# Kernel tuning notes

Hardware: AMD Instinct MI355X
Metric: run time of the kernel (lower is better)

## Reference

```python
import jax, jax.numpy as jnp
import numpy as np
from jax import lax

D_STATE = 16
D_CONV = 4
EXPAND = 2

def silu(x):
    return x * jax.nn.sigmoid(x)

def layernorm(x, w, b, eps=1e-5):
    mu = jnp.mean(x, axis=-1, keepdims=True)
    var = jnp.mean(jnp.square(x - mu), axis=-1, keepdims=True)
    return (x - mu) * lax.rsqrt(var + eps) * w + b

def adaln(x, t, W, b):
    # x: (B, N, C), t: (B, C); modulation = Linear(SiLU(t)) -> (B, 2C)
    m = silu(t) @ W.T + b
    scale, shift = jnp.split(m, 2, axis=-1)
    return x * (1.0 + scale[:, None, :]) + shift[:, None, :]

def mamba(x, W_in, conv_w, conv_b, W_x, W_dt, b_dt, A_log, D_p, W_out):
    # x: (B, L, D)
    B, L, D = x.shape
    di = conv_w.shape[0]           # d_inner = 2*D
    n = A_log.shape[1]             # d_state
    dtr = W_dt.shape[1]            # dt_rank
    xz = x @ W_in.T                # (B, L, 2*di)
    xi, z = jnp.split(xz, 2, axis=-1)
    # depthwise causal conv1d along L
    xt = jnp.transpose(xi, (0, 2, 1))                      # (B, di, L)
    xc = lax.conv_general_dilated(
        xt, conv_w[:, None, :], window_strides=(1,),
        padding=[(D_CONV - 1, 0)], feature_group_count=di,
        dimension_numbers=('NCH', 'OIH', 'NCH'))
    xc = silu(jnp.transpose(xc, (0, 2, 1)) + conv_b)       # (B, L, di)
    x_dbl = xc @ W_x.T                                     # (B, L, dtr+2n)
    dt, Bm, Cm = jnp.split(x_dbl, [dtr, dtr + n], axis=-1)
    delta = jax.nn.softplus(dt @ W_dt.T + b_dt)            # (B, L, di)
    A = -jnp.exp(A_log)                                    # (di, n)
    def step(h, inp):
        d_t, B_t, C_t, x_t = inp                           # (B,di),(B,n),(B,n),(B,di)
        dA = jnp.exp(d_t[..., None] * A)                   # (B, di, n)
        h = dA * h + (d_t * x_t)[..., None] * B_t[:, None, :]
        y = jnp.sum(h * C_t[:, None, :], axis=-1)          # (B, di)
        return h, y
    h0 = jnp.zeros((B, di, n), dtype=x.dtype)
    xs = (jnp.transpose(delta, (1, 0, 2)), jnp.transpose(Bm, (1, 0, 2)),
          jnp.transpose(Cm, (1, 0, 2)), jnp.transpose(xc, (1, 0, 2)))
    _, ys = lax.scan(step, h0, xs)                         # (L, B, di)
    y = jnp.transpose(ys, (1, 0, 2)) + xc * D_p
    y = y * silu(z)
    return y @ W_out.T

def _forward(query, diff_ts, p):
    outs = []
    n_layers = p['W_in'].shape[0]
    for i in range(n_layers):
        # cross-attn layer (Mamba) with AdaLN + residual + LN
        aq = adaln(query, diff_ts, p['attn_ada_W'][i], p['attn_ada_b'][i])
        attn = mamba(aq, p['W_in'][i], p['conv_w'][i], p['conv_b'][i],
                     p['W_x'][i], p['W_dt'][i], p['b_dt'][i],
                     p['A_log'][i], p['D_p'][i], p['W_out'][i])
        query = layernorm(query + attn, p['attn_ln_w'][i], p['attn_ln_b'][i])
        # FFN with AdaLN + residual + LN
        xf = adaln(query, diff_ts, p['ff_ada_W'][i], p['ff_ada_b'][i])
        h = jax.nn.relu(xf @ p['ff_W1'][i].T + p['ff_b1'][i])
        out = h @ p['ff_W2'][i].T + p['ff_b2'][i]
        query = layernorm(xf + out, p['ff_ln_w'][i], p['ff_ln_b'][i])
        outs.append(query)
    return tuple(outs)

def setup_inputs() -> dict:
    key = jax.random.key(0)
    B, L, D, NL = 4, 4096, 256, 4
    di = EXPAND * D
    n = D_STATE
    dtr = max(1, int(np.ceil(D / 16)))
    ks = iter(jax.random.split(key, 64))
    r = lambda shape, s=0.02: (s * jax.random.normal(next(ks), shape)).astype(jnp.float32)
    inp = {
        'query': jax.random.normal(next(ks), (B, L, D), dtype=jnp.float32),
        'value': jax.random.normal(next(ks), (B, L, D), dtype=jnp.float32),
        'diff_ts': jax.random.normal(next(ks), (B, D), dtype=jnp.float32),
        'W_in': r((NL, 2 * di, D)),
        'conv_w': r((NL, di, D_CONV), 0.2),
        'conv_b': r((NL, di)),
        'W_x': r((NL, dtr + 2 * n, di)),
        'W_dt': r((NL, di, dtr), 0.1),
        'b_dt': r((NL, di), 0.1),
        'A_log': jnp.log(jnp.broadcast_to(jnp.arange(1, n + 1, dtype=jnp.float32), (NL, di, n))),
        'D_p': jnp.ones((NL, di), dtype=jnp.float32),
        'W_out': r((NL, D, di)),
        'attn_ada_W': r((NL, 2 * D, D)),
        'attn_ada_b': r((NL, 2 * D)),
        'attn_ln_w': jnp.ones((NL, D), dtype=jnp.float32),
        'attn_ln_b': jnp.zeros((NL, D), dtype=jnp.float32),
        'ff_W1': r((NL, D, D)),
        'ff_b1': jnp.zeros((NL, D), dtype=jnp.float32),
        'ff_W2': r((NL, D, D)),
        'ff_b2': jnp.zeros((NL, D), dtype=jnp.float32),
        'ff_ln_w': jnp.ones((NL, D), dtype=jnp.float32),
        'ff_ln_b': jnp.zeros((NL, D), dtype=jnp.float32),
        'ff_ada_W': r((NL, 2 * D, D)),
        'ff_ada_b': r((NL, 2 * D)),
    }
    return inp

def reference(query, value, diff_ts, W_in, conv_w, conv_b, W_x, W_dt, b_dt,
              A_log, D_p, W_out, attn_ada_W, attn_ada_b, attn_ln_w, attn_ln_b,
              ff_W1, ff_b1, ff_W2, ff_b2, ff_ln_w, ff_ln_b, ff_ada_W, ff_ada_b):
    p = dict(W_in=W_in, conv_w=conv_w, conv_b=conv_b, W_x=W_x, W_dt=W_dt,
             b_dt=b_dt, A_log=A_log, D_p=D_p, W_out=W_out,
             attn_ada_W=attn_ada_W, attn_ada_b=attn_ada_b,
             attn_ln_w=attn_ln_w, attn_ln_b=attn_ln_b,
             ff_W1=ff_W1, ff_b1=ff_b1, ff_W2=ff_W2, ff_b2=ff_b2,
             ff_ln_w=ff_ln_w, ff_ln_b=ff_ln_b,
             ff_ada_W=ff_ada_W, ff_ada_b=ff_ada_b)
    return _forward(query, diff_ts, p)
```

## Files before the change

### kernel.cpp

```cpp
#include <hip/hip_runtime.h>
#include <hip/hip_bf16.h>

#define B_   4
#define L_   4096
#define D_   256
#define DI_  512
#define BL_  (B_*L_)
#define NL_  4
#define NC_  32
#define LC_  128

typedef __hip_bfloat16 bf16;
typedef __attribute__((ext_vector_type(8))) short short8;
typedef __attribute__((ext_vector_type(4))) short short4v;
typedef __attribute__((ext_vector_type(4))) float f32x4;

__device__ __forceinline__ float b2f(bf16 v) { return __bfloat162float(v); }
__device__ __forceinline__ float sh2f(short s) { bf16 h = *(bf16*)&s; return __bfloat162float(h); }
__device__ __forceinline__ float ldx(const void* p, size_t i, int isf32) {
  return isf32 ? ((const float*)p)[i] : b2f(((const bf16*)p)[i]);
}
__device__ __forceinline__ short f2s(float f) {
  bf16 h = __float2bfloat16(f);
  return *(short*)&h;
}

__global__ void k_probe(const unsigned* __restrict__ alog, int* __restrict__ flg) {
  if (threadIdx.x == 0) *flg = (alog[0] == 0u) ? 1 : 0;
}

__global__ __launch_bounds__(256) void k_cvt1(const void* __restrict__ src, size_t off,
                                              bf16* __restrict__ dst, int n,
                                              const int* __restrict__ flg) {
  int isf32 = *flg;
  int i = blockIdx.x * 256 + threadIdx.x;
  if (i < n) dst[i] = __float2bfloat16(ldx(src, off + i, isf32));
}

__global__ __launch_bounds__(256) void k_preA(const void* __restrict__ Alog,
                                              float* __restrict__ Ac,
                                              const int* __restrict__ flg) {
  int isf32 = *flg;
  int i = blockIdx.x * 256 + threadIdx.x;
  if (i < NL_ * 8192) Ac[i] = -__expf(ldx(Alog, (size_t)i, isf32)) * 1.44269504f;
}

__global__ __launch_bounds__(256) void k_mod(const void* __restrict__ t,
                                             const void* __restrict__ Wa, const void* __restrict__ ba,
                                             const void* __restrict__ Wf, const void* __restrict__ bfb,
                                             float* __restrict__ m,
                                             const int* __restrict__ flg) {
  int isf32 = *flg;
  int wt = blockIdx.x * 4 + (threadIdx.x >> 6);
  int lane = threadIdx.x & 63;
  int layer = wt >> 12;
  int w = wt & 4095;
  int o = w & 511;
  int b = (w >> 9) & 3;
  int which = w >> 11;
  const void* W  = which ? Wf : Wa;
  const void* bb = which ? bfb : ba;
  size_t wbase = (size_t)layer * 512 * 256 + (size_t)o * 256;
  float acc = 0.f;
#pragma unroll
  for (int j = 0; j < 4; ++j) {
    int k = lane + 64 * j;
    float tv = ldx(t, b * D_ + k, isf32);
    float s = tv / (1.f + __expf(-tv));
    acc = fmaf(s, ldx(W, wbase + k, isf32), acc);
  }
#pragma unroll
  for (int m2 = 32; m2 >= 1; m2 >>= 1) acc += __shfl_xor(acc, m2, 64);
  if (lane == 0) m[(layer << 12) + w] = acc + ldx(bb, (size_t)layer * 512 + o, isf32);
}

__global__ __launch_bounds__(256) void k_cvt_adaln(const void* __restrict__ qin,
                                                   bf16* __restrict__ q16,
                                                   bf16* __restrict__ oada,
                                                   const float* __restrict__ mod,
                                                   const int* __restrict__ flg) {
  int isf32 = *flg;
  int i = blockIdx.x * 256 + threadIdx.x;
  int c = i & (D_ - 1);
  int b = i >> 20;
  float v = ldx(qin, (size_t)i, isf32);
  q16[i] = __float2bfloat16(v);
  oada[i] = __float2bfloat16(fmaf(v, 1.f + mod[b * 512 + c], mod[b * 512 + 256 + c]));
}

__device__ __forceinline__ void gld_lds16(bf16* lds, const bf16* g) {
  __builtin_amdgcn_global_load_lds((const __attribute__((address_space(1))) unsigned int*)g,
                                   (__attribute__((address_space(3))) unsigned int*)lds,
                                   16, 0, 0);
}

__global__ __launch_bounds__(256) void k_gemm_t(const bf16* __restrict__ A,
                                                const bf16* __restrict__ W,
                                                const void* __restrict__ bias, size_t belem0,
                                                bf16* __restrict__ outB, bf16* __restrict__ out2,
                                                int N, int K, int relu,
                                                const int* __restrict__ flg) {
  __shared__ __align__(16) bf16 As[8192], Bs[8192];
  int isf32 = *flg;
  int tid = threadIdx.x;
  int lane = tid & 63, wave = tid >> 6;
  int tn = N >> 7;
  int m0 = (blockIdx.x / tn) << 7;
  int n0 = (blockIdx.x % tn) << 7;
  int wm = (wave >> 1) << 6, wn = (wave & 1) << 6;
  int r = lane & 15, q = lane >> 4;
  f32x4 acc[4][4];
#pragma unroll
  for (int a = 0; a < 4; ++a)
#pragma unroll
    for (int b = 0; b < 4; ++b) acc[a][b] = (f32x4){0.f, 0.f, 0.f, 0.f};
  const bf16* Ab = A + (size_t)m0 * K;
  const bf16* Wb = W + (size_t)n0 * K;
  for (int k0 = 0; k0 < K; k0 += 64) {
    __syncthreads();
#pragma unroll
    for (int j = 0; j < 4; ++j) {
      int g = tid + j * 256;
      int row = g >> 3;
      int slot = (g & 7) ^ (row & 7);
      gld_lds16(As + (size_t)g * 8, Ab + (size_t)row * K + k0 + slot * 8);
      gld_lds16(Bs + (size_t)g * 8, Wb + (size_t)row * K + k0 + slot * 8);
    }
    __syncthreads();
#pragma unroll
    for (int kk = 0; kk < 2; ++kk) {
      short8 af[4], bv[4];
#pragma unroll
      for (int f = 0; f < 4; ++f) {
        int ra = wm + f * 16 + r;
        af[f] = *(const short8*)((const short*)As + ra * 64 + (((kk * 4 + q) ^ (ra & 7)) << 3));
        int rb = wn + f * 16 + r;
        bv[f] = *(const short8*)((const short*)Bs + rb * 64 + (((kk * 4 + q) ^ (rb & 7)) << 3));
      }
#pragma unroll
      for (int i2 = 0; i2 < 4; ++i2)
#pragma unroll
        for (int j2 = 0; j2 < 4; ++j2)
          acc[i2][j2] = __builtin_amdgcn_mfma_f32_16x16x32_bf16(af[i2], bv[j2], acc[i2][j2], 0, 0, 0);
    }
  }
#pragma unroll
  for (int j2 = 0; j2 < 4; ++j2) {
    int col = n0 + wn + j2 * 16 + r;
    float bb = bias ? ldx(bias, belem0 + col, isf32) : 0.f;
#pragma unroll
    for (int i2 = 0; i2 < 4; ++i2) {
      int rw = m0 + wm + i2 * 16 + q * 4;
#pragma unroll
      for (int j = 0; j < 4; ++j) {
        float v = acc[i2][j2][j] + bb;
        if (relu) v = fmaxf(v, 0.f);
        bf16* dst; size_t idx;
        if (out2) {
          int hh = N >> 1;
          if (col < hh) { dst = outB; idx = (size_t)(rw + j) * hh + col; }
          else          { dst = out2; idx = (size_t)(rw + j) * hh + col - hh; }
        } else { dst = outB; idx = (size_t)(rw + j) * N + col; }
        dst[idx] = __float2bfloat16(v);
      }
    }
  }
}

__global__ __launch_bounds__(256) void k_gemm(const bf16* __restrict__ A,
                                              const bf16* __restrict__ W,
                                              bf16* __restrict__ outB,
                                              int N, int K) {
  int wave = threadIdx.x >> 6, lane = threadIdx.x & 63;
  int t = blockIdx.x * 4 + wave;
  int tn = N >> 4;
  int m0 = (t / tn) << 4;
  int n0 = (t % tn) << 4;
  int r = lane & 15, q = lane >> 4;
  const short* Ar = (const short*)A + (size_t)(m0 + r) * K + q * 8;
  const short* Wr = (const short*)W + (size_t)(n0 + r) * K + q * 8;
  f32x4 acc = {0.f, 0.f, 0.f, 0.f};
  for (int k = 0; k < K; k += 32)
    acc = __builtin_amdgcn_mfma_f32_16x16x32_bf16(*(const short8*)(Ar + k),
                                                  *(const short8*)(Wr + k), acc, 0, 0, 0);
  int col = n0 + r;
#pragma unroll
  for (int j = 0; j < 4; ++j)
    outB[(size_t)(m0 + q * 4 + j) * N + col] = __float2bfloat16(acc[j]);
}

__global__ __launch_bounds__(256) void k_conv(const bf16* __restrict__ Xi,
                                              const void* __restrict__ cw, const void* __restrict__ cb,
                                              bf16* __restrict__ xc16, int layer,
                                              const int* __restrict__ flg) {
  int isf32 = *flg;
  int i = blockIdx.x * 256 + threadIdx.x;
  int c8 = (i & 63) << 3;
  int row = i >> 6;
  int l = row & (L_ - 1);
  size_t cwb = (size_t)layer * 2048 + (size_t)c8 * 4;
  float acc[8];
#pragma unroll
  for (int e = 0; e < 8; ++e) acc[e] = ldx(cb, (size_t)layer * 512 + c8 + e, isf32);
#pragma unroll
  for (int j = 0; j < 4; ++j) {
    int ll = l - 3 + j;
    if (ll >= 0) {
      short8 xv = *(const short8*)((const short*)Xi + (size_t)(row - 3 + j) * 512 + c8);
#pragma unroll
      for (int e = 0; e < 8; ++e) {
        acc[e] = fmaf(ldx(cw, cwb + e * 4 + j, isf32), sh2f(xv[e]), acc[e]);
      }
    }
  }
  short8 o;
#pragma unroll
  for (int e = 0; e < 8; ++e) {
    float s = acc[e] * (1.f / (1.f + __expf(-acc[e])));
    o[e] = f2s(s);
  }
  *(short8*)((short*)xc16 + (size_t)row * 512 + c8) = o;
}

__global__ __launch_bounds__(256) void k_xpose(const bf16* __restrict__ src,
                                               bf16* __restrict__ dst) {
  __shared__ bf16 t[64][66];
  int bid = blockIdx.x;
  int ct = bid & 7;
  int lt = (bid >> 3) & 63;
  int b  = bid >> 9;
  int l0 = lt * 64, c0 = ct * 64;
  int tx = threadIdx.x & 63;
  int ty = threadIdx.x >> 6;
#pragma unroll
  for (int j = 0; j < 16; ++j) {
    int l = ty + j * 4;
    t[l][tx] = src[(size_t)(b * L_ + l0 + l) * 512 + c0 + tx];
  }
  __syncthreads();
#pragma unroll
  for (int j = 0; j < 16; ++j) {
    int c = ty + j * 4;
    dst[(size_t)(b * 512 + c0 + c) * L_ + l0 + tx] = t[tx][c];
  }
}

__global__ __launch_bounds__(256) void k_scan1_t(const bf16* __restrict__ Tx,
                                                 const bf16* __restrict__ xdbl,
                                                 const void* __restrict__ Wdt,
                                                 const void* __restrict__ bdt,
                                                 const float* __restrict__ Ac, int layer,
                                                 bf16* __restrict__ Pscr, float* __restrict__ Hscr,
                                                 const int* __restrict__ flg) {
  __shared__ __align__(16) bf16 rowbuf[LC_ * 48];
  __shared__ bf16 dlbuf[64 * 130];
  int isf32 = *flg;
  int tid = blockIdx.x * 256 + threadIdx.x;
  int nh = tid & 3;
  int d  = (tid >> 2) & 511;
  int t2 = tid >> 11;
  int c  = t2 & (NC_ - 1);
  int b  = t2 >> 5;
  int dl = (threadIdx.x >> 2) & 63;
  const bf16* rowg = xdbl + (size_t)(b * L_ + c * LC_) * 48;
#pragma unroll
  for (int j = 0; j < 3; ++j) {
    int o = threadIdx.x * 8 + j * 2048;
    *(short8*)(rowbuf + o) = *(const short8*)(rowg + o);
  }
  __syncthreads();
  {
    float w[16];
    size_t wb = (size_t)layer * 8192 + (size_t)d * 16;
#pragma unroll
    for (int k = 0; k < 16; ++k) w[k] = ldx(Wdt, wb + k, isf32);
    float dbias = ldx(bdt, (size_t)layer * 512 + d, isf32);
    for (int jl = 0; jl < 32; ++jl) {
      int l = nh * 32 + jl;
      const bf16* rr = rowbuf + l * 48;
      short8 t0 = *(const short8*)rr;
      short8 t1 = *(const short8*)(rr + 8);
      float acc = dbias;
#pragma unroll
      for (int k = 0; k < 8; ++k) acc = fmaf(sh2f(t0[k]), w[k], acc);
#pragma unroll
      for (int k = 0; k < 8; ++k) acc = fmaf(sh2f(t1[k]), w[k + 8], acc);
      dlbuf[dl * 130 + l] = __float2bfloat16(fmaxf(acc, 0.f) + log1pf(__expf(-fabsf(acc))));
    }
  }
  __syncthreads();
  const float* ap = Ac + (size_t)layer * 8192 + (size_t)d * 16 + nh * 4;
  float av[4], h[4], P[4];
#pragma unroll
  for (int n = 0; n < 4; ++n) { av[n] = ap[n]; h[n] = 0.f; P[n] = 1.f; }
  const bf16* xp = Tx + (size_t)(b * 512 + d) * L_ + c * LC_;
  const bf16* dlp = dlbuf + dl * 130;
  for (int l8 = 0; l8 < LC_; l8 += 8) {
    short8 xv8 = *(const short8*)(xp + l8);
#pragma unroll
    for (int e = 0; e < 8; ++e) {
      int l = l8 + e;
      float dv = b2f(dlp[l]);
      short4v bm = *(const short4v*)(rowbuf + l * 48 + 16 + nh * 4);
      float u = dv * sh2f(xv8[e]);
#pragma unroll
      for (int n = 0; n < 4; ++n) {
        float da = exp2f(dv * av[n]);
        h[n] = fmaf(da, h[n], u * sh2f(bm[n]));
        P[n] *= da;
      }
    }
  }
  int s = (b * 512 + d) * 16 + nh * 4;
  bf16* pp = Pscr + (size_t)c * 32768 + s;
  float* hp = Hscr + (size_t)c * 32768 + s;
#pragma unroll
  for (int n = 0; n < 4; ++n) { pp[n] = __float2bfloat16(P[n]); hp[n] = h[n]; }
}

__global__ __launch_bounds__(256) void k_scan2(const bf16* __restrict__ Pscr,
                                               float* __restrict__ Hscr) {
  int s = blockIdx.x * 256 + threadIdx.x;
  float hin = 0.f;
  for (int c = 0; c < NC_; ++c) {
    float P  = b2f(Pscr[(size_t)c * 32768 + s]);
    float he = Hscr[(size_t)c * 32768 + s];
    Hscr[(size_t)c * 32768 + s] = hin;
    hin = fmaf(P, hin, he);
  }
}

__global__ __launch_bounds__(256) void k_scan3_t(bf16* __restrict__ Tx,
                                                 const bf16* __restrict__ xdbl,
                                                 const void* __restrict__ Wdt,
                                                 const void* __restrict__ bdt,
                                                 const float* __restrict__ Ac, int layer,
                                                 const float* __restrict__ Hscr,
                                                 const int* __restrict__ flg) {
  __shared__ __align__(16) bf16 rowbuf[LC_ * 48];
  __shared__ bf16 dlbuf[64 * 130];
  int isf32 = *flg;
  int tid = blockIdx.x * 256 + threadIdx.x;
  int nh = tid & 3;
  int d  = (tid >> 2) & 511;
  int t2 = tid >> 11;
  int c  = t2 & (NC_ - 1);
  int b  = t2 >> 5;
  int dl = (threadIdx.x >> 2) & 63;
  const bf16* rowg = xdbl + (size_t)(b * L_ + c * LC_) * 48;
#pragma unroll
  for (int j = 0; j < 3; ++j) {
    int o = threadIdx.x * 8 + j * 2048;
    *(short8*)(rowbuf + o) = *(const short8*)(rowg + o);
  }
  __syncthreads();
  {
    float w[16];
    size_t wb = (size_t)layer * 8192 + (size_t)d * 16;
#pragma unroll
    for (int k = 0; k < 16; ++k) w[k] = ldx(Wdt, wb + k, isf32);
    float dbias = ldx(bdt, (size_t)layer * 512 + d, isf32);
    for (int jl = 0; jl < 32; ++jl) {
      int l = nh * 32 + jl;
      const bf16* rr = rowbuf + l * 48;
      short8 t0 = *(const short8*)rr;
      short8 t1 = *(const short8*)(rr + 8);
      float acc = dbias;
#pragma unroll
      for (int k = 0; k < 8; ++k) acc = fmaf(sh2f(t0[k]), w[k], acc);
#pragma unroll
      for (int k = 0; k < 8; ++k) acc = fmaf(sh2f(t1[k]), w[k + 8], acc);
      dlbuf[dl * 130 + l] = __float2bfloat16(fmaxf(acc, 0.f) + log1pf(__expf(-fabsf(acc))));
    }
  }
  __syncthreads();
  const float* ap = Ac + (size_t)layer * 8192 + (size_t)d * 16 + nh * 4;
  int s = (b * 512 + d) * 16 + nh * 4;
  const float* hp = Hscr + (size_t)c * 32768 + s;
  float av[4], h[4];
#pragma unroll
  for (int n = 0; n < 4; ++n) { av[n] = ap[n]; h[n] = hp[n]; }
  bf16* xp = Tx + (size_t)(b * 512 + d) * L_ + c * LC_;
  const bf16* dlp = dlbuf + dl * 130;
  for (int l8 = 0; l8 < LC_; l8 += 8) {
    short8 xv8 = *(const short8*)(xp + l8);
    short8 y8;
#pragma unroll
    for (int e = 0; e < 8; ++e) {
      int l = l8 + e;
      float dv = b2f(dlp[l]);
      short4v bm = *(const short4v*)(rowbuf + l * 48 + 16 + nh * 4);
      short4v cm = *(const short4v*)(rowbuf + l * 48 + 32 + nh * 4);
      float u = dv * sh2f(xv8[e]);
      float y = 0.f;
#pragma unroll
      for (int n = 0; n < 4; ++n) {
        float da = exp2f(dv * av[n]);
        h[n] = fmaf(da, h[n], u * sh2f(bm[n]));
        y = fmaf(h[n], sh2f(cm[n]), y);
      }
      y += __shfl_xor(y, 1, 64);
      y += __shfl_xor(y, 2, 64);
      y8[e] = f2s(y);
    }
    if (nh == 0) *(short8*)(xp + l8) = y8;
  }
}

__global__ __launch_bounds__(256) void k_gate_t(const bf16* __restrict__ yT,
                                                bf16* __restrict__ xc,
                                                const bf16* __restrict__ Z,
                                                const void* __restrict__ Dp, int layer,
                                                const int* __restrict__ flg) {
  __shared__ bf16 t[64][66];
  int isf32 = *flg;
  int bid = blockIdx.x;
  int ct = bid & 7;
  int lt = (bid >> 3) & 63;
  int b  = bid >> 9;
  int l0 = lt * 64, c0 = ct * 64;
  int tx = threadIdx.x & 63;
  int ty = threadIdx.x >> 6;
#pragma unroll
  for (int j = 0; j < 16; ++j) {
    int dd = ty + j * 4;
    t[dd][tx] = yT[(size_t)(b * 512 + c0 + dd) * L_ + l0 + tx];
  }
  __syncthreads();
  float dpv = ldx(Dp, (size_t)layer * 512 + c0 + tx, isf32);
#pragma unroll
  for (int j = 0; j < 16; ++j) {
    int l = ty + j * 4;
    size_t row = (size_t)(b * L_ + l0 + l);
    float y  = b2f(t[tx][l]);
    float xcv = b2f(xc[row * 512 + c0 + tx]);
    float zv = b2f(Z[row * 512 + c0 + tx]);
    float v = fmaf(xcv, dpv, y);
    xc[row * 512 + c0 + tx] = __float2bfloat16(v * zv / (1.f + __expf(-zv)));
  }
}

__global__ __launch_bounds__(256) void k_delta(const bf16* __restrict__ xdbl,
                                               const void* __restrict__ Wdt, const void* __restrict__ bdt,
                                               bf16* __restrict__ dly, int layer,
                                               const int* __restrict__ flg) {
  __shared__ float Wls[256 * 17];
  int isf32 = *flg;
  int i = blockIdx.x * 256 + threadIdx.x;
  int d = i & (DI_ - 1);
  int row = i >> 9;
  int d0 = (blockIdx.x & 1) * 256;
  size_t wbase = (size_t)layer * 512 * 16 + (size_t)d0 * 16;
#pragma unroll
  for (int jj = 0; jj < 16; ++jj) {
    int j = threadIdx.x + jj * 256;
    Wls[(j >> 4) * 17 + (j & 15)] = ldx(Wdt, wbase + j, isf32);
  }
  __syncthreads();
  float acc = ldx(bdt, (size_t)layer * 512 + d, isf32);
  const bf16* dt = xdbl + (size_t)row * 48;
  const float* wrow = Wls + (size_t)(d - d0) * 17;
#pragma unroll
  for (int k = 0; k < 16; ++k) acc = fmaf(b2f(dt[k]), wrow[k], acc);
  float sp = fmaxf(acc, 0.f) + log1pf(__expf(-fabsf(acc)));
  dly[(size_t)row * 512 + d] = __float2bfloat16(sp);
}

__global__ __launch_bounds__(256) void k_scan(const bf16* __restrict__ dly,
                                              bf16* __restrict__ xc,
                                              const bf16* __restrict__ Z,
                                              const bf16* __restrict__ xdbl,
                                              const void* __restrict__ Alog,
                                              const void* __restrict__ Dp,
                                              int layer, const int* __restrict__ flg) {
  int tid = blockIdx.x * 256 + threadIdx.x;
  int n = tid & 15;
  int d = (tid >> 4) & (DI_ - 1);
  int b = tid >> 13;
  int isf32 = *flg;
  float a_c = -__expf(ldx(Alog, (size_t)layer * 8192 + d * 16 + n, isf32));
  float dpv = ldx(Dp, (size_t)layer * 512 + d, isf32);
  const bf16* drow = dly + (size_t)b * L_ * 512 + d;
  bf16* grow = xc + (size_t)b * L_ * 512 + d;
  const bf16* zrow = Z + (size_t)b * L_ * 512 + d;
  const bf16* brow = xdbl + (size_t)b * L_ * 48 + 16 + n;
  const bf16* crow = brow + 16;
  float h = 0.f;
  for (int l = 0; l < L_; ++l) {
    float dv = b2f(drow[(size_t)l * 512]);
    float xv = b2f(grow[(size_t)l * 512]);
    float bm = b2f(brow[(size_t)l * 48]);
    float cm = b2f(crow[(size_t)l * 48]);
    float da = __expf(dv * a_c);
    h = fmaf(da, h, dv * xv * bm);
    float p = h * cm;
    p += __shfl_xor(p, 1, 64);
    p += __shfl_xor(p, 2, 64);
    p += __shfl_xor(p, 4, 64);
    p += __shfl_xor(p, 8, 64);
    if (n == 0) {
      float zv = b2f(zrow[(size_t)l * 512]);
      float v = fmaf(xv, dpv, p);
      grow[(size_t)l * 512] = __float2bfloat16(v * zv / (1.f + __expf(-zv)));
    }
  }
}

__global__ __launch_bounds__(256) void k_resln(const bf16* __restrict__ xa,
                                               const bf16* __restrict__ xb,
                                               const void* __restrict__ w, const void* __restrict__ bias,
                                               bf16* __restrict__ oq, float* __restrict__ o32,
                                               const float* __restrict__ mod, bf16* __restrict__ oada,
                                               int layer, const int* __restrict__ flg) {
  int isf32 = *flg;
  int row = blockIdx.x;
  int c = threadIdx.x;
  int i = row * D_ + c;
  float v = b2f(xa[i]) + b2f(xb[i]);
  float s = v, s2 = v * v;
#pragma unroll
  for (int m = 32; m >= 1; m >>= 1) {
    s  += __shfl_xor(s, m, 64);
    s2 += __shfl_xor(s2, m, 64);
  }
  __shared__ float ps[4], ps2[4];
  int wave = threadIdx.x >> 6;
  if ((threadIdx.x & 63) == 0) { ps[wave] = s; ps2[wave] = s2; }
  __syncthreads();
  s  = ps[0] + ps[1] + ps[2] + ps[3];
  s2 = ps2[0] + ps2[1] + ps2[2] + ps2[3];
  float mu = s * (1.f / D_);
  float var = s2 * (1.f / D_) - mu * mu;
  float rs = rsqrtf(var + 1e-5f);
  float o = (v - mu) * rs * ldx(w, (size_t)layer * 256 + c, isf32)
          + ldx(bias, (size_t)layer * 256 + c, isf32);
  oq[i] = __float2bfloat16(o);
  if (o32) o32[i] = o;
  if (mod) {
    int b = row >> 12;
    oada[i] = __float2bfloat16(fmaf(o, 1.f + mod[b * 512 + c], mod[b * 512 + 256 + c]));
  }
}

extern "C" void kernel_launch(void* const* d_in, const int* in_sizes, int n_in,
                              void* d_out, int out_size, void* d_ws, size_t ws_size,
                              hipStream_t stream) {
  const void* query   = d_in[0];
  const void* diff_ts = d_in[2];
  const void* W_in    = d_in[3];
  const void* conv_w  = d_in[4];
  const void* conv_b  = d_in[5];
  const void* W_x     = d_in[6];
  const void* W_dt    = d_in[7];
  const void* b_dt    = d_in[8];
  const void* A_log   = d_in[9];
  const void* D_p     = d_in[10];
  const void* W_out   = d_in[11];
  const void* adaW_a  = d_in[12];
  const void* adab_a  = d_in[13];
  const void* lnw_a   = d_in[14];
  const void* lnb_a   = d_in[15];
  const void* ff_W1   = d_in[16];
  const void* ff_b1   = d_in[17];
  const void* ff_W2   = d_in[18];
  const void* ff_b2   = d_in[19];
  const void* lnw_f   = d_in[20];
  const void* lnb_f   = d_in[21];
  const void* adaW_f  = d_in[22];
  const void* adab_f  = d_in[23];
  float* dout = (float*)d_out;

  if (in_sizes[0] != BL_ * D_ || in_sizes[3] != NL_ * 1024 * 256 ||
      in_sizes[9] != NL_ * 512 * 16 || in_sizes[11] != NL_ * 256 * 512) return;

  const size_t BL = BL_;
  bf16* q16   = (bf16*)d_ws;
  bf16* R1    = q16 + BL * 256;
  bf16* Xi    = R1 + BL * 512;
  bf16* Zb    = Xi + BL * 512;
  bf16* xdbl  = Zb + BL * 512;
  float* mball = (float*)(xdbl + BL * 48);
  int* dflag  = (int*)(mball + NL_ * 4096);
  char* cur   = (char*)(dflag + 8);

  const size_t s_in = 262144, s_x = 24576, s_o = 131072, s_1 = 65536, s_2 = 65536;
  const size_t seg_sum = s_in + s_x + s_o + s_1 + s_2;
  const size_t scanbytes = (size_t)NC_ * 32768 * 6 + (size_t)NL_ * 8192 * 4;

  if (ws_size < (size_t)(cur - (char*)d_ws) + seg_sum * 2) return;
  size_t have = ws_size - (size_t)(cur - (char*)d_ws);

  bf16* Pscr = nullptr; float* Hscr = nullptr; float* Acoef = nullptr; int tr = 0;
  if (have >= scanbytes + seg_sum * 2) {
    Pscr = (bf16*)cur;
    Hscr = (float*)(Pscr + (size_t)NC_ * 32768);
    Acoef = Hscr + (size_t)NC_ * 32768;
    cur  = (char*)(Acoef + (size_t)NL_ * 8192);
    have -= scanbytes;
    tr = 1;
  }
  int full_cache = have >= seg_sum * 2 * NL_;
  size_t f = full_cache ? NL_ : 1;
  bf16* Wb_in = (bf16*)cur;
  bf16* Wb_x  = Wb_in + s_in * f;
  bf16* Wb_o  = Wb_x  + s_x * f;
  bf16* Wb_1  = Wb_o  + s_o * f;
  bf16* Wb_2  = Wb_1  + s_1 * f;

  bf16* att16 = Xi;
  bf16* h16   = Xi + BL * 256;
  bf16* ffo16 = Zb;

  k_probe<<<1, 64, 0, stream>>>((const unsigned*)A_log, dflag);
  k_mod<<<4096, 256, 0, stream>>>(diff_ts, adaW_a, adab_a, adaW_f, adab_f, mball, dflag);
  if (tr) k_preA<<<128, 256, 0, stream>>>(A_log, Acoef, dflag);
  if (full_cache) {
    k_cvt1<<<(int)((s_in * NL_ + 255) / 256), 256, 0, stream>>>(W_in, 0, Wb_in, (int)(s_in * NL_), dflag);
    k_cvt1<<<(int)((s_x  * NL_ + 255) / 256), 256, 0, stream>>>(W_x,  0, Wb_x,  (int)(s_x  * NL_), dflag);
    k_cvt1<<<(int)((s_o  * NL_ + 255) / 256), 256, 0, stream>>>(W_out,0, Wb_o,  (int)(s_o  * NL_), dflag);
    k_cvt1<<<(int)((s_1  * NL_ + 255) / 256), 256, 0, stream>>>(ff_W1,0, Wb_1,  (int)(s_1  * NL_), dflag);
    k_cvt1<<<(int)((s_2  * NL_ + 255) / 256), 256, 0, stream>>>(ff_W2,0, Wb_2,  (int)(s_2  * NL_), dflag);
  }
  k_cvt_adaln<<<16384, 256, 0, stream>>>(query, q16, R1, mball, dflag);

  for (int i = 0; i < NL_; ++i) {
    size_t ob = (size_t)i * 256;
    size_t wi = full_cache ? (size_t)i : 0;
    if (!full_cache) {
      k_cvt1<<<(int)((s_in + 255) / 256), 256, 0, stream>>>(W_in,  (size_t)i * s_in, Wb_in, (int)s_in, dflag);
      k_cvt1<<<(int)((s_x  + 255) / 256), 256, 0, stream>>>(W_x,   (size_t)i * s_x,  Wb_x,  (int)s_x,  dflag);
      k_cvt1<<<(int)((s_o  + 255) / 256), 256, 0, stream>>>(W_out, (size_t)i * s_o,  Wb_o,  (int)s_o,  dflag);
      k_cvt1<<<(int)((s_1  + 255) / 256), 256, 0, stream>>>(ff_W1, (size_t)i * s_1,  Wb_1,  (int)s_1,  dflag);
      k_cvt1<<<(int)((s_2  + 255) / 256), 256, 0, stream>>>(ff_W2, (size_t)i * s_2,  Wb_2,  (int)s_2,  dflag);
    }
    k_gemm_t<<<1024, 256, 0, stream>>>(R1, Wb_in + wi * s_in, nullptr, 0,
                                       Xi, Zb, 1024, 256, 0, dflag);
    k_conv<<<4096, 256, 0, stream>>>(Xi, conv_w, conv_b, R1, i, dflag);
    k_gemm<<<768, 256, 0, stream>>>(R1, Wb_x + wi * s_x, xdbl, 48, 512);
    if (tr) {
      k_xpose<<<2048, 256, 0, stream>>>(R1, Xi);
      k_scan1_t<<<1024, 256, 0, stream>>>(Xi, xdbl, W_dt, b_dt, Acoef, i, Pscr, Hscr, dflag);
      k_scan2<<<128, 256, 0, stream>>>(Pscr, Hscr);
      k_scan3_t<<<1024, 256, 0, stream>>>(Xi, xdbl, W_dt, b_dt, Acoef, i, Hscr, dflag);
      k_gate_t<<<2048, 256, 0, stream>>>(Xi, R1, Zb, D_p, i, dflag);
    } else {
      k_delta<<<32768, 256, 0, stream>>>(xdbl, W_dt, b_dt, Xi, i, dflag);
      k_scan<<<128, 256, 0, stream>>>(Xi, R1, Zb, xdbl, A_log, D_p, i, dflag);
    }
    k_gemm_t<<<256, 256, 0, stream>>>(R1, Wb_o + wi * s_o, nullptr, 0,
                                      att16, nullptr, 256, 512, 0, dflag);
    k_resln<<<16384, 256, 0, stream>>>(q16, att16, lnw_a, lnb_a, q16, nullptr,
                                       mball + i * 4096 + 2048, R1, i, dflag);
    k_gemm_t<<<256, 256, 0, stream>>>(R1, Wb_1 + wi * s_1, ff_b1, ob,
                                      h16, nullptr, 256, 256, 1, dflag);
    k_gemm_t<<<256, 256, 0, stream>>>(h16, Wb_2 + wi * s_2, ff_b2, ob,
                                      ffo16, nullptr, 256, 256, 0, dflag);
    k_resln<<<16384, 256, 0, stream>>>(R1, ffo16, lnw_f, lnb_f, q16, dout + (size_t)i * (BL * 256),
                                       (i < NL_ - 1) ? mball + (i + 1) * 4096 : nullptr, R1, i, dflag);
  }
}
```

Baseline: 1.698 ms.

## Fuse chunked scan passes into one cooperative kernel with grid sync

Merges the three chunked selective-scan kernels into one cooperative kernel. After the per-chunk pass it does a grid-wide sync, and each chunk then recomputes its incoming state serially from the saved chunk products and states. This avoids recomputing delta and reloading the rows in a second kernel, and removes two launches per layer. Chunk decay products are now fp32, taken as exp2 of A times the summed delta instead of a running product, and softplus uses fast log. The cost is a prefix loop over prior chunks that grows with chunk index, and the need for all 1024 blocks to be co-resident, with fallback to the old path otherwise.

```diff
diff --git a/kernel.cpp b/kernel.cpp
--- a/kernel.cpp
+++ b/kernel.cpp
@@ -1,5 +1,6 @@
 #include <hip/hip_runtime.h>
 #include <hip/hip_bf16.h>
+#include <hip/hip_cooperative_groups.h>
 
 #define B_   4
 #define L_   4096
@@ -23,6 +24,9 @@
 __device__ __forceinline__ short f2s(float f) {
   bf16 h = __float2bfloat16(f);
   return *(short*)&h;
+}
+__device__ __forceinline__ float softplus_f(float x) {
+  return fmaxf(x, 0.f) + __logf(1.f + __expf(-fabsf(x)));
 }
 
 __global__ void k_probe(const unsigned* __restrict__ alog, int* __restrict__ flg) {
@@ -245,13 +249,13 @@
   }
 }
 
-__global__ __launch_bounds__(256) void k_scan1_t(const bf16* __restrict__ Tx,
-                                                 const bf16* __restrict__ xdbl,
-                                                 const void* __restrict__ Wdt,
-                                                 const void* __restrict__ bdt,
-                                                 const float* __restrict__ Ac, int layer,
-                                                 bf16* __restrict__ Pscr, float* __restrict__ Hscr,
-                                                 const int* __restrict__ flg) {
+__global__ __launch_bounds__(256) void k_scan_f(bf16* __restrict__ Tx,
+                                                const bf16* __restrict__ xdbl,
+                                                const void* __restrict__ Wdt,
+                                                const void* __restrict__ bdt,
+                                                const float* __restrict__ Ac, int layer,
+                                                float* __restrict__ Pscr, float* __restrict__ Hscr,
+                                                const int* __restrict__ flg) {
   __shared__ __align__(16) bf16 rowbuf[LC_ * 48];
   __shared__ bf16 dlbuf[64 * 130];
   int isf32 = *flg;
@@ -276,7 +280,7 @@
     for (int k = 0; k < 16; ++k) w[k] = ldx(Wdt, wb + k, isf32);
     float dbias = ldx(bdt, (size_t)layer * 512 + d, isf32);
     for (int jl = 0; jl < 32; ++jl) {
-      int l = nh * 32 + jl;
+      int l = jl * 4 + nh;
       const bf16* rr = rowbuf + l * 48;
       short8 t0 = *(const short8*)rr;
       short8 t1 = *(const short8*)(rr + 8);
@@ -285,14 +289,124 @@
       for (int k = 0; k < 8; ++k) acc = fmaf(sh2f(t0[k]), w[k], acc);
 #pragma unroll
       for (int k = 0; k < 8; ++k) acc = fmaf(sh2f(t1[k]), w[k + 8], acc);
-      dlbuf[dl * 130 + l] = __float2bfloat16(fmaxf(acc, 0.f) + log1pf(__expf(-fabsf(acc))));
+      dlbuf[dl * 130 + l] = __float2bfloat16(softplus_f(acc));
     }
   }
   __syncthreads();
   const float* ap = Ac + (size_t)layer * 8192 + (size_t)d * 16 + nh * 4;
-  float av[4], h[4], P[4];
-#pragma unroll
-  for (int n = 0; n < 4; ++n) { av[n] = ap[n]; h[n] = 0.f; P[n] = 1.f; }
+  float av[4], h[4];
+#pragma unroll
+  for (int n = 0; n < 4; ++n) { av[n] = ap[n]; h[n] = 0.f; }
+  float sdv = 0.f;
+  bf16* xp = Tx + (size_t)(b * 512 + d) * L_ + c * LC_;
+  const bf16* dlp = dlbuf + dl * 130;
+  for (int l8 = 0; l8 < LC_; l8 += 8) {
+    short8 xv8 = *(const short8*)(xp + l8);
+#pragma unroll
+    for (int e = 0; e < 8; ++e) {
+      int l = l8 + e;
+      float dv = b2f(dlp[l]);
+      short4v bm = *(const short4v*)(rowbuf + l * 48 + 16 + nh * 4);
+      sdv += dv;
+      float u = dv * sh2f(xv8[e]);
+#pragma unroll
+      for (int n = 0; n < 4; ++n) {
+        float da = exp2f(dv * av[n]);
+        h[n] = fmaf(da, h[n], u * sh2f(bm[n]));
+      }
+    }
+  }
+  int s = (b * 512 + d) * 16 + nh * 4;
+  f32x4 Pv, Hv;
+#pragma unroll
+  for (int n = 0; n < 4; ++n) { Pv[n] = exp2f(av[n] * sdv); Hv[n] = h[n]; }
+  *(f32x4*)(Pscr + (size_t)c * 32768 + s) = Pv;
+  *(f32x4*)(Hscr + (size_t)c * 32768 + s) = Hv;
+  __threadfence();
+  cooperative_groups::this_grid().sync();
+  f32x4 hin = {0.f, 0.f, 0.f, 0.f};
+  for (int c2 = 0; c2 < c; ++c2) {
+    f32x4 P = *(const f32x4*)(Pscr + (size_t)c2 * 32768 + s);
+    f32x4 H = *(const f32x4*)(Hscr + (size_t)c2 * 32768 + s);
+#pragma unroll
+    for (int n = 0; n < 4; ++n) hin[n] = fmaf(P[n], hin[n], H[n]);
+  }
+#pragma unroll
+  for (int n = 0; n < 4; ++n) h[n] = hin[n];
+  for (int l8 = 0; l8 < LC_; l8 += 8) {
+    short8 xv8 = *(const short8*)(xp + l8);
+    short8 y8;
+#pragma unroll
+    for (int e = 0; e < 8; ++e) {
+      int l = l8 + e;
+      float dv = b2f(dlp[l]);
+      short4v bm = *(const short4v*)(rowbuf + l * 48 + 16 + nh * 4);
+      short4v cm = *(const short4v*)(rowbuf + l * 48 + 32 + nh * 4);
+      float u = dv * sh2f(xv8[e]);
+      float y = 0.f;
+#pragma unroll
+      for (int n = 0; n < 4; ++n) {
+        float da = exp2f(dv * av[n]);
+        h[n] = fmaf(da, h[n], u * sh2f(bm[n]));
+        y = fmaf(h[n], sh2f(cm[n]), y);
+      }
+      y += __shfl_xor(y, 1, 64);
+      y += __shfl_xor(y, 2, 64);
+      y8[e] = f2s(y);
+    }
+    if (nh == 0) *(short8*)(xp + l8) = y8;
+  }
+}
+
+__global__ __launch_bounds__(256) void k_scan1_t(const bf16* __restrict__ Tx,
+                                                 const bf16* __restrict__ xdbl,
+                                                 const void* __restrict__ Wdt,
+                                                 const void* __restrict__ bdt,
+                                                 const float* __restrict__ Ac, int layer,
+                                                 float* __restrict__ Pscr, float* __restrict__ Hscr,
+                                                 const int* __restrict__ flg) {
+  __shared__ __align__(16) bf16 rowbuf[LC_ * 48];
+  __shared__ bf16 dlbuf[64 * 130];
+  int isf32 = *flg;
+  int tid = blockIdx.x * 256 + threadIdx.x;
+  int nh = tid & 3;
+  int d  = (tid >> 2) & 511;
+  int t2 = tid >> 11;
+  int c  = t2 & (NC_ - 1);
+  int b  = t2 >> 5;
+  int dl = (threadIdx.x >> 2) & 63;
+  const bf16* rowg = xdbl + (size_t)(b * L_ + c * LC_) * 48;
+#pragma unroll
+  for (int j = 0; j < 3; ++j) {
+    int o = threadIdx.x * 8 + j * 2048;
+    *(short8*)(rowbuf + o) = *(const short8*)(rowg + o);
+  }
+  __syncthreads();
+  {
+    float w[16];
+    size_t wb = (size_t)layer * 8192 + (size_t)d * 16;
+#pragma unroll
+    for (int k = 0; k < 16; ++k) w[k] = ldx(Wdt, wb + k, isf32);
+    float dbias = ldx(bdt, (size_t)layer * 512 + d, isf32);
+    for (int jl = 0; jl < 32; ++jl) {
+      int l = jl * 4 + nh;
+      const bf16* rr = rowbuf + l * 48;
+      short8 t0 = *(const short8*)rr;
+      short8 t1 = *(const short8*)(rr + 8);
+      float acc = dbias;
+#pragma unroll
+      for (int k = 0; k < 8; ++k) acc = fmaf(sh2f(t0[k]), w[k], acc);
+#pragma unroll
+      for (int k = 0; k < 8; ++k) acc = fmaf(sh2f(t1[k]), w[k + 8], acc);
+      dlbuf[dl * 130 + l] = __float2bfloat16(softplus_f(acc));
+    }
+  }
+  __syncthreads();
+  const float* ap = Ac + (size_t)layer * 8192 + (size_t)d * 16 + nh * 4;
+  float av[4], h[4];
+#pragma unroll
+  for (int n = 0; n < 4; ++n) { av[n] = ap[n]; h[n] = 0.f; }
+  float sdv = 0.f;
   const bf16* xp = Tx + (size_t)(b * 512 + d) * L_ + c * LC_;
   const bf16* dlp = dlbuf + dl * 130;
   for (int l8 = 0; l8 < LC_; l8 += 8) {
@@ -302,28 +416,29 @@
       int l = l8 + e;
       float dv = b2f(dlp[l]);
       short4v bm = *(const short4v*)(rowbuf + l * 48 + 16 + nh * 4);
+      sdv += dv;
       float u = dv * sh2f(xv8[e]);
 #pragma unroll
       for (int n = 0; n < 4; ++n) {
         float da = exp2f(dv * av[n]);
         h[n] = fmaf(da, h[n], u * sh2f(bm[n]));
-        P[n] *= da;
       }
     }
   }
   int s = (b * 512 + d) * 16 + nh * 4;
-  bf16* pp = Pscr + (size_t)c * 32768 + s;
-  float* hp = Hscr + (size_t)c * 32768 + s;
-#pragma unroll
-  for (int n = 0; n < 4; ++n) { pp[n] = __float2bfloat16(P[n]); hp[n] = h[n]; }
-}
-
-__global__ __launch_bounds__(256) void k_scan2(const bf16* __restrict__ Pscr,
+  f32x4 Pv, Hv;
+#pragma unroll
+  for (int n = 0; n < 4; ++n) { Pv[n] = exp2f(av[n] * sdv); Hv[n] = h[n]; }
+  *(f32x4*)(Pscr + (size_t)c * 32768 + s) = Pv;
+  *(f32x4*)(Hscr + (size_t)c * 32768 + s) = Hv;
+}
+
+__global__ __launch_bounds__(256) void k_scan2(const float* __restrict__ Pscr,
                                                float* __restrict__ Hscr) {
   int s = blockIdx.x * 256 + threadIdx.x;
   float hin = 0.f;
   for (int c = 0; c < NC_; ++c) {
-    float P  = b2f(Pscr[(size_t)c * 32768 + s]);
+    float P  = Pscr[(size_t)c * 32768 + s];
     float he = Hscr[(size_t)c * 32768 + s];
     Hscr[(size_t)c * 32768 + s] = hin;
     hin = fmaf(P, hin, he);
@@ -361,7 +476,7 @@
     for (int k = 0; k < 16; ++k) w[k] = ldx(Wdt, wb + k, isf32);
     float dbias = ldx(bdt, (size_t)layer * 512 + d, isf32);
     for (int jl = 0; jl < 32; ++jl) {
-      int l = nh * 32 + jl;
+      int l = jl * 4 + nh;
       const bf16* rr = rowbuf + l * 48;
       short8 t0 = *(const short8*)rr;
       short8 t1 = *(const short8*)(rr + 8);
@@ -370,7 +485,7 @@
       for (int k = 0; k < 8; ++k) acc = fmaf(sh2f(t0[k]), w[k], acc);
 #pragma unroll
       for (int k = 0; k < 8; ++k) acc = fmaf(sh2f(t1[k]), w[k + 8], acc);
-      dlbuf[dl * 130 + l] = __float2bfloat16(fmaxf(acc, 0.f) + log1pf(__expf(-fabsf(acc))));
+      dlbuf[dl * 130 + l] = __float2bfloat16(softplus_f(acc));
     }
   }
   __syncthreads();
@@ -585,15 +700,15 @@
 
   const size_t s_in = 262144, s_x = 24576, s_o = 131072, s_1 = 65536, s_2 = 65536;
   const size_t seg_sum = s_in + s_x + s_o + s_1 + s_2;
-  const size_t scanbytes = (size_t)NC_ * 32768 * 6 + (size_t)NL_ * 8192 * 4;
+  const size_t scanbytes = (size_t)NC_ * 32768 * 8 + (size_t)NL_ * 8192 * 4;
 
   if (ws_size < (size_t)(cur - (char*)d_ws) + seg_sum * 2) return;
   size_t have = ws_size - (size_t)(cur - (char*)d_ws);
 
-  bf16* Pscr = nullptr; float* Hscr = nullptr; float* Acoef = nullptr; int tr = 0;
+  float* Pscr = nullptr; float* Hscr = nullptr; float* Acoef = nullptr; int tr = 0;
   if (have >= scanbytes + seg_sum * 2) {
-    Pscr = (bf16*)cur;
-    Hscr = (float*)(Pscr + (size_t)NC_ * 32768);
+    Pscr = (float*)cur;
+    Hscr = Pscr + (size_t)NC_ * 32768;
     Acoef = Hscr + (size_t)NC_ * 32768;
     cur  = (char*)(Acoef + (size_t)NL_ * 8192);
     have -= scanbytes;
@@ -606,6 +721,14 @@
   bf16* Wb_o  = Wb_x  + s_x * f;
   bf16* Wb_1  = Wb_o  + s_o * f;
   bf16* Wb_2  = Wb_1  + s_1 * f;
+
+  int coop = 0;
+  if (tr) {
+    int nb = 0;
+    if (hipOccupancyMaxActiveBlocksPerMultiprocessor(&nb, (const void*)k_scan_f, 256, 0) == hipSuccess
+        && nb >= 4)
+      coop = 1;
+  }
 
   bf16* att16 = Xi;
   bf16* h16   = Xi + BL * 256;
@@ -639,9 +762,22 @@
     k_gemm<<<768, 256, 0, stream>>>(R1, Wb_x + wi * s_x, xdbl, 48, 512);
     if (tr) {
       k_xpose<<<2048, 256, 0, stream>>>(R1, Xi);
-      k_scan1_t<<<1024, 256, 0, stream>>>(Xi, xdbl, W_dt, b_dt, Acoef, i, Pscr, Hscr, dflag);
-      k_scan2<<<128, 256, 0, stream>>>(Pscr, Hscr);
-      k_scan3_t<<<1024, 256, 0, stream>>>(Xi, xdbl, W_dt, b_dt, Acoef, i, Hscr, dflag);
+      int launched = 0;
+      if (coop) {
+        bf16* TxP = Xi; const bf16* xdP = xdbl;
+        const void* WdtP = W_dt; const void* bdtP = b_dt;
+        const float* AcP = Acoef; int li = i;
+        float* PsP = Pscr; float* HsP = Hscr; const int* fgP = dflag;
+        void* ka[] = {&TxP, &xdP, &WdtP, &bdtP, &AcP, &li, &PsP, &HsP, &fgP};
+        if (hipLaunchCooperativeKernel((const void*)k_scan_f, dim3(1024), dim3(256),
+                                       ka, 0, stream) == hipSuccess)
+          launched = 1;
+      }
+      if (!launched) {
+        k_scan1_t<<<1024, 256, 0, stream>>>(Xi, xdbl, W_dt, b_dt, Acoef, i, Pscr, Hscr, dflag);
+        k_scan2<<<128, 256, 0, stream>>>(Pscr, Hscr);
+        k_scan3_t<<<1024, 256, 0, stream>>>(Xi, xdbl, W_dt, b_dt, Acoef, i, Hscr, dflag);
+      }
       k_gate_t<<<2048, 256, 0, stream>>>(Xi, R1, Zb, D_p, i, dflag);
     } else {
       k_delta<<<32768, 256, 0, stream>>>(xdbl, W_dt, b_dt, Xi, i, dflag);
```

Result: faster. 1.531 ms (-9.9%).
